# Optimization experiments

Hardware: AMD Instinct MI355X
Metric: run time of the kernel (lower is better)

The kernel has to match this reference:

```python
import jax, jax.numpy as jnp
import numpy as np

B, T, D = 2, 2048, 2048
HK, HV, K, V = 16, 32, 128, 128          # key heads, value heads, head dims
KEY_DIM, VALUE_DIM = HK * K, HV * V      # 2048, 4096
CONV_W = 4                               # causal conv kernel width
EPS = 1e-6


def setup_inputs() -> dict:
    key = jax.random.key(0)
    ks = jax.random.split(key, 8)
    rn = lambda k, shp, sc: jax.random.normal(k, shp, dtype=jnp.float32) * sc
    return {
        "hidden_states": rn(ks[0], (B, T, D), 1.0),
        "W_qkvz": rn(ks[1], (D, 2 * KEY_DIM + 2 * VALUE_DIM), D ** -0.5),
        "W_ba": rn(ks[2], (D, 2 * HV), D ** -0.5),
        "conv_weight": rn(ks[3], (2 * KEY_DIM + VALUE_DIM, CONV_W), CONV_W ** -0.5),
        "A_log": jnp.log(jax.random.uniform(ks[4], (HV,), minval=1.0, maxval=16.0)),
        "dt_bias": rn(ks[5], (HV,), 0.5),
        "norm_weight": jnp.zeros((V,), jnp.float32),  # zero-centered RMSNorm weight
        "W_out": rn(ks[6], (VALUE_DIM, D), VALUE_DIM ** -0.5),
    }


def _l2norm(x):
    return x * jax.lax.rsqrt(jnp.sum(x * x, axis=-1, keepdims=True) + 1e-6)


def _causal_conv_silu(x, w):
    # x: [B,T,C]; depthwise causal conv, kernel width CONV_W, then SiLU
    xp = jnp.pad(x, ((0, 0), (CONV_W - 1, 0), (0, 0)))
    out = sum(xp[:, j:j + x.shape[1], :] * w[None, None, :, j] for j in range(CONV_W))
    return jax.nn.silu(out)


def _gated_delta_rule(q, k, v, g, beta):
    # q,k: [B,T,HV,K] (l2-normed, q pre-scaled); v: [B,T,HV,V]; g,beta: [B,T,HV]
    def step(S, xs):                      # S: [B,HV,K,V]
        q_t, k_t, v_t, g_t, beta_t = xs
        S = S * jnp.exp(g_t)[..., None, None]
        pred = jnp.einsum('bhk,bhkv->bhv', k_t, S)
        delta = (v_t - pred) * beta_t[..., None]
        S = S + jnp.einsum('bhk,bhv->bhkv', k_t, delta)
        o_t = jnp.einsum('bhk,bhkv->bhv', q_t, S)
        return S, o_t

    mv = lambda x: jnp.moveaxis(x, 1, 0)  # time-major for scan
    S0 = jnp.zeros((q.shape[0], HV, K, V), q.dtype)
    _, o = jax.lax.scan(step, S0, (mv(q), mv(k), mv(v), mv(g), mv(beta)))
    return jnp.moveaxis(o, 0, 1)          # [B,T,HV,V]


def reference(hidden_states, W_qkvz, W_ba, conv_weight, A_log, dt_bias,
              norm_weight, W_out):
    b_, t_ = hidden_states.shape[:2]
    qkvz = hidden_states @ W_qkvz
    q, k, v, z = jnp.split(qkvz, [KEY_DIM, 2 * KEY_DIM, 2 * KEY_DIM + VALUE_DIM], axis=-1)
    ba = hidden_states @ W_ba
    b_gate, a = jnp.split(ba, 2, axis=-1)  # each [B,T,HV]

    # fused causal conv1d + SiLU over concat(q,k,v)
    mixed = _causal_conv_silu(jnp.concatenate([q, k, v], axis=-1), conv_weight)
    q, k, v = jnp.split(mixed, [KEY_DIM, 2 * KEY_DIM], axis=-1)

    # gating: beta = sigmoid(b), g = -exp(A_log) * softplus(a + dt_bias)
    beta = jax.nn.sigmoid(b_gate)
    g = -jnp.exp(A_log) * jax.nn.softplus(a + dt_bias)

    # GQA expand (v_per_k_group = HV // HK), l2norm, scale
    rep = HV // HK
    q = jnp.repeat(q.reshape(b_, t_, HK, K), rep, axis=2)
    k = jnp.repeat(k.reshape(b_, t_, HK, K), rep, axis=2)
    v = v.reshape(b_, t_, HV, V)
    q = _l2norm(q) * (K ** -0.5)
    k = _l2norm(k)

    o = _gated_delta_rule(q, k, v, g, beta)  # [B,T,HV,V]

    # gated RMSNorm (per value head, zero-centered weight) then out projection
    zg = z.reshape(b_, t_, HV, V)
    x = o * jax.nn.silu(zg)
    var = jnp.mean(x * x, axis=-1, keepdims=True)
    x = x * jax.lax.rsqrt(var + EPS) * (1.0 + norm_weight)
    return x.reshape(b_, t_, VALUE_DIM) @ W_out
```

## Files before the change

### kernel.cpp

```cpp
#include <hip/hip_runtime.h>

typedef unsigned short u16;
typedef unsigned int u32;

typedef short bf16x8 __attribute__((ext_vector_type(8)));
typedef float f32x4 __attribute__((ext_vector_type(4)));

#define T_SEQ 2048
#define MFMA16(a, b, c) __builtin_amdgcn_mfma_f32_16x16x32_bf16(a, b, c, 0, 0, 0)

__device__ __forceinline__ u16 f2bf(float f) {
    u32 u = __float_as_uint(f);
    u += 0x7fffu + ((u >> 16) & 1u);
    return (u16)(u >> 16);
}
__device__ __forceinline__ float bf2f(u16 s) {
    return __uint_as_float(((u32)s) << 16);
}
__device__ __forceinline__ void g2lds16(const u16* gp, u16* lp) {
    __builtin_amdgcn_global_load_lds((const __attribute__((address_space(1))) void*)gp,
                                     (__attribute__((address_space(3))) void*)lp, 16, 0, 0);
}

__global__ __launch_bounds__(256) void cast_f32_bf16(const float* __restrict__ in,
                                                     u16* __restrict__ out, long n) {
    long i = ((long)blockIdx.x * 256 + threadIdx.x) * 4;
    if (i + 3 < n) {
        float4 v = *(const float4*)&in[i];
        out[i + 0] = f2bf(v.x);
        out[i + 1] = f2bf(v.y);
        out[i + 2] = f2bf(v.z);
        out[i + 3] = f2bf(v.w);
    }
}

__global__ __launch_bounds__(256) void transpose_cast(const float* __restrict__ in,
                                                      u16* __restrict__ out, int R, int C) {
    __shared__ float tile[32][33];
    int c0 = blockIdx.x * 32, r0 = blockIdx.y * 32;
    int tx = threadIdx.x & 31, ty = threadIdx.x >> 5;
#pragma unroll
    for (int rr = 0; rr < 32; rr += 8)
        tile[ty + rr][tx] = in[(long)(r0 + ty + rr) * C + c0 + tx];
    __syncthreads();
#pragma unroll
    for (int rr = 0; rr < 32; rr += 8)
        out[(long)(c0 + ty + rr) * R + r0 + tx] = f2bf(tile[tx][ty + rr]);
}

template <int MODE>
__global__ __launch_bounds__(256) void gemm_bt(const u16* __restrict__ A,
                                               const u16* __restrict__ B, void* __restrict__ C,
                                               void* __restrict__ C2, int M, int N, int K, int lda,
                                               int ldb, int ldc) {
    __shared__ __align__(16) u16 As[128 * 32];
    __shared__ __align__(16) u16 Bs[128 * 32];
    int m0 = blockIdx.x * 128, n0 = blockIdx.y * 128;
    int tid = threadIdx.x;
    int lane = tid & 63, w = tid >> 6;
    int wr = w >> 1, wc = w & 1;
    int quad = lane >> 4, l15 = lane & 15;

    f32x4 acc[4][4];
#pragma unroll
    for (int i = 0; i < 4; i++)
#pragma unroll
        for (int j = 0; j < 4; j++) acc[i][j] = (f32x4){0.f, 0.f, 0.f, 0.f};

    int srow = tid >> 2, sc8 = (tid & 3) * 8;
    const u16* Ag = &A[(long)(m0 + srow) * lda + sc8];
    const u16* Bg = &B[(long)(n0 + srow) * ldb + sc8];

    for (int k0 = 0; k0 < K; k0 += 32) {
        g2lds16(Ag + k0, &As[tid * 8]);
        g2lds16(Ag + (long)64 * lda + k0, &As[(256 + tid) * 8]);
        g2lds16(Bg + k0, &Bs[tid * 8]);
        g2lds16(Bg + (long)64 * ldb + k0, &Bs[(256 + tid) * 8]);
        __syncthreads();
        bf16x8 af[4], bfr[4];
#pragma unroll
        for (int i = 0; i < 4; i++) {
            af[i] = *(const bf16x8*)&As[(wr * 64 + i * 16 + l15) * 32 + quad * 8];
            bfr[i] = *(const bf16x8*)&Bs[(wc * 64 + i * 16 + l15) * 32 + quad * 8];
        }
#pragma unroll
        for (int i = 0; i < 4; i++)
#pragma unroll
            for (int j = 0; j < 4; j++) acc[i][j] = MFMA16(af[i], bfr[j], acc[i][j]);
        __syncthreads();
    }

    if (MODE == 0) {
#pragma unroll
        for (int i = 0; i < 4; i++)
#pragma unroll
            for (int j = 0; j < 4; j++)
#pragma unroll
                for (int r = 0; r < 4; r++) {
                    int row = m0 + wr * 64 + i * 16 + quad * 4 + r;
                    int col = n0 + wc * 64 + j * 16 + l15;
                    ((float*)C)[(long)row * ldc + col] = acc[i][j][r];
                }
    } else {
        u16* Cst = As;
        u16* dst;
        long dldc;
        int ncol0;
        if (MODE == 2 && n0 >= 8192) {
            dst = (u16*)C2;
            dldc = 4096;
            ncol0 = n0 - 8192;
        } else {
            dst = (u16*)C;
            dldc = (MODE == 2) ? 8192 : ldc;
            ncol0 = n0;
        }
#pragma unroll 1
        for (int half = 0; half < 2; half++) {
            __syncthreads();
            if (wc == half) {
#pragma unroll
                for (int i = 0; i < 4; i++)
#pragma unroll
                    for (int j = 0; j < 4; j++)
#pragma unroll
                        for (int r = 0; r < 4; r++) {
                            int row = wr * 64 + i * 16 + quad * 4 + r;
                            int col = j * 16 + l15;
                            u16* base = (row < 64) ? As : Bs;
                            base[(row & 63) * 64 + col] = f2bf(acc[i][j][r]);
                        }
            }
            __syncthreads();
#pragma unroll
            for (int rr = 0; rr < 4; rr++) {
                int row = rr * 32 + (tid >> 3), seg = tid & 7;
                u16* base = (row < 64) ? As : Bs;
                *(uint4*)&dst[(long)(m0 + row) * dldc + ncol0 + half * 64 + seg * 8] =
                    *(uint4*)&base[(row & 63) * 64 + seg * 8];
            }
        }
    }
}

__global__ __launch_bounds__(256) void ba_gemm(const u16* __restrict__ hid,
                                               const u16* __restrict__ WbaT,
                                               const float* __restrict__ A_log,
                                               const float* __restrict__ dt_bias,
                                               float* __restrict__ g, float* __restrict__ beta) {
    __shared__ __align__(16) u16 As2[32 * 32];
    int m0 = blockIdx.x * 32;
    int tid = threadIdx.x, lane = tid & 63, w = tid >> 6;
    int quad = lane >> 4, l15 = lane & 15;
    int trow = w & 1;
    int ctile = (w >> 1) * 2;
    f32x4 acc[2];
    acc[0] = (f32x4){0.f, 0.f, 0.f, 0.f};
    acc[1] = (f32x4){0.f, 0.f, 0.f, 0.f};
    for (int k0 = 0; k0 < 2048; k0 += 32) {
        if (tid < 128) {
            int row = tid >> 2, c8 = (tid & 3) * 8;
            *(uint4*)&As2[row * 32 + c8] = *(const uint4*)&hid[(long)(m0 + row) * 2048 + k0 + c8];
        }
        __syncthreads();
        bf16x8 a = *(const bf16x8*)&As2[(trow * 16 + l15) * 32 + quad * 8];
#pragma unroll
        for (int j = 0; j < 2; j++) {
            bf16x8 b = *(const bf16x8*)&WbaT[(long)((ctile + j) * 16 + l15) * 2048 + k0 + quad * 8];
            acc[j] = MFMA16(a, b, acc[j]);
        }
        __syncthreads();
    }
#pragma unroll
    for (int j = 0; j < 2; j++)
#pragma unroll
        for (int r = 0; r < 4; r++) {
            int tok = m0 + trow * 16 + quad * 4 + r;
            int col = (ctile + j) * 16 + l15;
            float tot = acc[j][r];
            if (col < 32) {
                beta[(long)tok * 32 + col] = 1.f / (1.f + expf(-tot));
            } else {
                int h = col - 32;
                float x = tot + dt_bias[h];
                float sp = (x > 20.f) ? x : log1pf(expf(x));
                g[(long)tok * 32 + h] = -expf(A_log[h]) * sp;
            }
        }
}

__global__ __launch_bounds__(256) void conv_gate(const u16* __restrict__ qkv,
                                                 const float* __restrict__ conv_w,
                                                 u16* __restrict__ qn, u16* __restrict__ kn,
                                                 u16* __restrict__ vc) {
    int tok = blockIdx.x, tid = threadIdx.x;
    int tloc = tok & (T_SEQ - 1);
    __shared__ float mixed[8192];
    __shared__ float sh_norm[32];
    uint4 zero4;
    zero4.x = zero4.y = zero4.z = zero4.w = 0u;
#pragma unroll
    for (int i = 0; i < 4; i++) {
        int c = (i * 256 + tid) * 8;
        long base = (long)tok * 8192 + c;
        uint4 x3 = *(const uint4*)&qkv[base];
        uint4 x2 = (tloc >= 1) ? *(const uint4*)&qkv[base - 8192] : zero4;
        uint4 x1 = (tloc >= 2) ? *(const uint4*)&qkv[base - 16384] : zero4;
        uint4 x0 = (tloc >= 3) ? *(const uint4*)&qkv[base - 24576] : zero4;
        const u16* p0 = (const u16*)&x0;
        const u16* p1 = (const u16*)&x1;
        const u16* p2 = (const u16*)&x2;
        const u16* p3 = (const u16*)&x3;
#pragma unroll
        for (int e = 0; e < 8; e++) {
            float4 wv = *(const float4*)&conv_w[(long)(c + e) * 4];
            float a = bf2f(p0[e]) * wv.x + bf2f(p1[e]) * wv.y + bf2f(p2[e]) * wv.z +
                      bf2f(p3[e]) * wv.w;
            mixed[c + e] = a / (1.f + __expf(-a));
        }
    }
    __syncthreads();
    int grp = tid >> 3, sub = tid & 7;
    float ss = 0.f;
#pragma unroll
    for (int e = 0; e < 16; e++) {
        float v = mixed[grp * 128 + sub * 16 + e];
        ss += v * v;
    }
    ss += __shfl_xor(ss, 4, 8);
    ss += __shfl_xor(ss, 2, 8);
    ss += __shfl_xor(ss, 1, 8);
    if (sub == 0) sh_norm[grp] = rsqrtf(ss + 1e-6f);
    __syncthreads();
#pragma unroll
    for (int i = 0; i < 4; i++) {
        int c = (i * 256 + tid) * 8;
        float nf = (c < 2048) ? sh_norm[c >> 7] * 0.08838834764831845f
                              : ((c < 4096) ? sh_norm[c >> 7] : 1.f);
        u16 ob[8];
#pragma unroll
        for (int e = 0; e < 8; e++) ob[e] = f2bf(mixed[c + e] * nf);
        uint4 val = *(uint4*)ob;
        if (c < 2048)
            *(uint4*)&qn[(long)tok * 2048 + c] = val;
        else if (c < 4096)
            *(uint4*)&kn[(long)tok * 2048 + (c - 2048)] = val;
        else
            *(uint4*)&vc[(long)tok * 4096 + (c - 4096)] = val;
    }
}

__global__ __launch_bounds__(256) void phaseA(const u16* __restrict__ qn,
                                              const u16* __restrict__ kn,
                                              const u16* __restrict__ vc,
                                              const float* __restrict__ g,
                                              const float* __restrict__ beta,
                                              u16* __restrict__ Tv_g, u16* __restrict__ Tw_g,
                                              u16* __restrict__ Q2_g, u16* __restrict__ obuf) {
    __shared__ __align__(16) u16 Yrm[64][256];
    __shared__ __align__(16) float BMt[64][64];
    __shared__ __align__(16) u16 kbuf[64][128];
    u16* Lbf = &kbuf[0][0];

    int bid = blockIdx.x;
    int c = bid & 31, h = (bid >> 5) & 31, b = bid >> 10;
    int hk = h >> 1;
    long tokbase = (long)b * T_SEQ + c * 64;
    long cb = (long)bid * 8192;
    int tid = threadIdx.x, lane = tid & 63, w = tid >> 6;
    int quad = lane >> 4, l15 = lane & 15;

    float gl = g[(tokbase + lane) * 32 + h];
    float bl = beta[(tokbase + lane) * 32 + h];
    float cgl = gl;
#pragma unroll
    for (int d = 1; d < 64; d <<= 1) {
        float y = __shfl_up(cgl, d);
        if (lane >= d) cgl += y;
    }
    float wscl = bl * __expf(cgl);
    float eCgl = __expf(cgl);

#pragma unroll
    for (int p = 0; p < 4; p++) {
        int u = p * 256 + tid;
        int row = u >> 4, col8 = (u & 15) * 8;
        *(uint4*)&kbuf[row][col8] = *(const uint4*)&kn[(tokbase + row) * 2048 + hk * 128 + col8];
    }
    __syncthreads();

    {
        f32x4 gk[4];
#pragma unroll
        for (int nj = 0; nj < 4; nj++) gk[nj] = (f32x4){0.f, 0.f, 0.f, 0.f};
#pragma unroll
        for (int kk = 0; kk < 4; kk++) {
            bf16x8 a = *(const bf16x8*)&kbuf[w * 16 + l15][kk * 32 + quad * 8];
#pragma unroll
            for (int nj = 0; nj < 4; nj++) {
                bf16x8 bb = *(const bf16x8*)&kbuf[nj * 16 + l15][kk * 32 + quad * 8];
                gk[nj] = MFMA16(a, bb, gk[nj]);
            }
        }
#pragma unroll
        for (int nj = 0; nj < 4; nj++)
#pragma unroll
            for (int r = 0; r < 4; r++) {
                int i = w * 16 + quad * 4 + r;
                int j = nj * 16 + l15;
                float cgi = __shfl(cgl, i), cgj = __shfl(cgl, j);
                float bi = __shfl(bl, i);
                BMt[j][i] = (j < i) ? bi * gk[nj][r] * __expf(cgi - cgj) : 0.f;
            }
    }
    __syncthreads();

    {
        int col = tid;
        bool isV = col < 128;
        int kcol = col & 127;
        long vbase = tokbase * 4096 + h * 128 + kcol;
        float Yreg[8], acc8[8];
#pragma unroll 1
        for (int bi = 0; bi < 8; ++bi) {
            float vr[8];
            if (isV) {
#pragma unroll
                for (int ii = 0; ii < 8; ii++)
                    vr[ii] = bf2f(vc[vbase + (long)(bi * 8 + ii) * 4096]);
            }
#pragma unroll
            for (int ii = 0; ii < 8; ii++) acc8[ii] = 0.f;
            for (int j = 0; j < bi * 8; ++j) {
                float yv = bf2f(Yrm[j][col]);
                float4 m0 = *(const float4*)&BMt[j][bi * 8];
                float4 m1 = *(const float4*)&BMt[j][bi * 8 + 4];
                acc8[0] += m0.x * yv;
                acc8[1] += m0.y * yv;
                acc8[2] += m0.z * yv;
                acc8[3] += m0.w * yv;
                acc8[4] += m1.x * yv;
                acc8[5] += m1.y * yv;
                acc8[6] += m1.z * yv;
                acc8[7] += m1.w * yv;
            }
#pragma unroll
            for (int ii = 0; ii < 8; ii++) {
                int i = bi * 8 + ii;
                float rhs = isV ? __shfl(bl, i) * vr[ii] : __shfl(wscl, i) * bf2f(kbuf[i][kcol]);
                float s = rhs - acc8[ii];
#pragma unroll
                for (int jj = 0; jj < 8; jj++)
                    if (jj < ii) s -= BMt[bi * 8 + jj][i] * Yreg[jj];
                Yreg[ii] = s;
                u16 sb = f2bf(s);
                Yrm[i][col] = sb;
                if (isV)
                    Tv_g[cb + i * 128 + kcol] = sb;
                else
                    Tw_g[cb + i * 128 + kcol] = sb;
            }
        }
    }
    __syncthreads();

    {
        f32x4 qk_[4];
#pragma unroll
        for (int nj = 0; nj < 4; nj++) qk_[nj] = (f32x4){0.f, 0.f, 0.f, 0.f};
#pragma unroll
        for (int kk = 0; kk < 4; kk++) {
            bf16x8 a = *(const bf16x8*)&qn[(tokbase + w * 16 + l15) * 2048 + hk * 128 + kk * 32 +
                                           quad * 8];
#pragma unroll
            for (int nj = 0; nj < 4; nj++) {
                bf16x8 bb = *(const bf16x8*)&kbuf[nj * 16 + l15][kk * 32 + quad * 8];
                qk_[nj] = MFMA16(a, bb, qk_[nj]);
            }
        }
        __syncthreads();
#pragma unroll
        for (int nj = 0; nj < 4; nj++)
#pragma unroll
            for (int r = 0; r < 4; r++) {
                int t = w * 16 + quad * 4 + r;
                int rr = nj * 16 + l15;
                float cgt = __shfl(cgl, t), cgr = __shfl(cgl, rr);
                float val = (rr <= t) ? qk_[nj][r] * __expf(cgt - cgr) : 0.f;
                Lbf[t * 64 + rr] = f2bf(val);
            }
    }
    __syncthreads();

#pragma unroll 1
    for (int half = 0; half < 2; half++) {
        f32x4 oa[8];
#pragma unroll
        for (int nj = 0; nj < 8; nj++) oa[nj] = (f32x4){0.f, 0.f, 0.f, 0.f};
#pragma unroll
        for (int kk = 0; kk < 2; kk++) {
            bf16x8 a = *(const bf16x8*)&Lbf[(w * 16 + l15) * 64 + kk * 32 + quad * 8];
#pragma unroll
            for (int nj = 0; nj < 8; nj++) {
                bf16x8 bb;
#pragma unroll
                for (int jj = 0; jj < 8; jj++)
                    bb[jj] = (short)Yrm[kk * 32 + quad * 8 + jj][half * 128 + nj * 16 + l15];
                oa[nj] = MFMA16(a, bb, oa[nj]);
            }
        }
        if (half == 0) {
#pragma unroll
            for (int nj = 0; nj < 8; nj++)
#pragma unroll
                for (int r = 0; r < 4; r++) {
                    int t = w * 16 + quad * 4 + r;
                    int vcol = nj * 16 + l15;
                    obuf[(tokbase + t) * 4096 + h * 128 + vcol] = f2bf(oa[nj][r]);
                }
        } else {
#pragma unroll
            for (int nj = 0; nj < 8; nj++)
#pragma unroll
                for (int r = 0; r < 4; r++) {
                    int t = w * 16 + quad * 4 + r;
                    int kcol = nj * 16 + l15;
                    float qsc = __shfl(eCgl, t);
                    float qv = bf2f(qn[(tokbase + t) * 2048 + hk * 128 + kcol]);
                    Q2_g[cb + t * 128 + kcol] = f2bf(qsc * qv - oa[nj][r]);
                }
        }
    }
}

__global__ __launch_bounds__(256) void phaseB(const u16* __restrict__ kn,
                                              const float* __restrict__ g,
                                              const u16* __restrict__ Tv_g,
                                              const u16* __restrict__ Tw_g,
                                              const u16* __restrict__ Q2_g,
                                              u16* __restrict__ obuf) {
    __shared__ __align__(16) float Sf[128][32];
    __shared__ __align__(16) u16 SbfT[32][128];
    __shared__ __align__(16) u16 KhT[128][64];
    __shared__ __align__(16) u16 Ut[32][64];

    int bid = blockIdx.x;
    int vq = bid & 3, h = (bid >> 2) & 31, b = bid >> 7;
    int hk = h >> 1;
    int tid = threadIdx.x, lane = tid & 63, w = tid >> 6;
    int quad = lane >> 4, l15 = lane & 15;

    for (int p = tid; p < 128 * 32; p += 256) {
        ((float*)Sf)[p] = 0.f;
        ((u16*)SbfT)[p] = 0;
    }
    __syncthreads();

    for (int c = 0; c < 32; ++c) {
        long tokbase = (long)b * T_SEQ + c * 64;
        long cb = (long)(((b * 32 + h) * 32) + c) * 8192;
        float gl = g[(tokbase + lane) * 32 + h];
        float cgl = gl;
#pragma unroll
        for (int d = 1; d < 64; d <<= 1) {
            float y = __shfl_up(cgl, d);
            if (lane >= d) cgl += y;
        }
        float cgC = __shfl(cgl, 63);
        float A_C = __expf(cgC);
        float kscl = __expf(cgC - cgl);

        {
            int s = tid >> 2, qq = tid & 3;
            float ksc = __shfl(kscl, s);
            const u16* kp = &kn[(tokbase + s) * 2048 + hk * 128 + qq * 32];
            u16 tmp[32];
            *(uint4*)&tmp[0] = *(const uint4*)&kp[0];
            *(uint4*)&tmp[8] = *(const uint4*)&kp[8];
            *(uint4*)&tmp[16] = *(const uint4*)&kp[16];
            *(uint4*)&tmp[24] = *(const uint4*)&kp[24];
#pragma unroll
            for (int j = 0; j < 32; j++) KhT[qq * 32 + j][s] = f2bf(bf2f(tmp[j]) * ksc);
        }

        f32x4 y1[2], oo[2];
#pragma unroll
        for (int nj = 0; nj < 2; nj++) {
            y1[nj] = (f32x4){0.f, 0.f, 0.f, 0.f};
            oo[nj] = (f32x4){0.f, 0.f, 0.f, 0.f};
        }
#pragma unroll
        for (int kk = 0; kk < 4; kk++) {
            bf16x8 aTw = *(const bf16x8*)&Tw_g[cb + (w * 16 + l15) * 128 + kk * 32 + quad * 8];
            bf16x8 aQ2 = *(const bf16x8*)&Q2_g[cb + (w * 16 + l15) * 128 + kk * 32 + quad * 8];
#pragma unroll
            for (int nj = 0; nj < 2; nj++) {
                bf16x8 bb = *(const bf16x8*)&SbfT[nj * 16 + l15][kk * 32 + quad * 8];
                y1[nj] = MFMA16(aTw, bb, y1[nj]);
                oo[nj] = MFMA16(aQ2, bb, oo[nj]);
            }
        }
#pragma unroll
        for (int nj = 0; nj < 2; nj++)
#pragma unroll
            for (int r = 0; r < 4; r++) {
                int i = w * 16 + quad * 4 + r;
                int vl = nj * 16 + l15;
                int vg = vq * 32 + vl;
                float tvv = bf2f(Tv_g[cb + (long)i * 128 + vg]);
                Ut[vl][i] = f2bf(tvv - y1[nj][r]);
                long op = (tokbase + i) * 4096 + h * 128 + vg;
                obuf[op] = f2bf(bf2f(obuf[op]) + oo[nj][r]);
            }
        __syncthreads();

#pragma unroll
        for (int mm = 0; mm < 2; mm++) {
            int mi = 2 * w + mm;
#pragma unroll
            for (int nj = 0; nj < 2; nj++) {
                f32x4 sacc;
#pragma unroll
                for (int r = 0; r < 4; r++)
                    sacc[r] = A_C * Sf[mi * 16 + quad * 4 + r][nj * 16 + l15];
#pragma unroll
                for (int kk = 0; kk < 2; kk++) {
                    bf16x8 a = *(const bf16x8*)&KhT[mi * 16 + l15][kk * 32 + quad * 8];
                    bf16x8 bb = *(const bf16x8*)&Ut[nj * 16 + l15][kk * 32 + quad * 8];
                    sacc = MFMA16(a, bb, sacc);
                }
#pragma unroll
                for (int r = 0; r < 4; r++) {
                    int kd = mi * 16 + quad * 4 + r, vl = nj * 16 + l15;
                    Sf[kd][vl] = sacc[r];
                    SbfT[vl][kd] = f2bf(sacc[r]);
                }
            }
        }
        __syncthreads();
    }
}

__global__ __launch_bounds__(256) void gated_norm(const u16* __restrict__ obuf,
                                                  const u16* __restrict__ zbuf,
                                                  const float* __restrict__ norm_w,
                                                  u16* __restrict__ xn) {
    int tok = blockIdx.x, tid = threadIdx.x;
    long obase = (long)tok * 4096 + tid * 16;
    u16 ob[16], zb[16];
    *(uint4*)(ob + 0) = *(const uint4*)&obuf[obase];
    *(uint4*)(ob + 8) = *(const uint4*)&obuf[obase + 8];
    *(uint4*)(zb + 0) = *(const uint4*)&zbuf[obase];
    *(uint4*)(zb + 8) = *(const uint4*)&zbuf[obase + 8];
    float x[16];
    float ss = 0.f;
#pragma unroll
    for (int i = 0; i < 16; i++) {
        float ov = bf2f(ob[i]);
        float zv = bf2f(zb[i]);
        float xv = ov * (zv / (1.f + expf(-zv)));
        x[i] = xv;
        ss += xv * xv;
    }
    ss += __shfl_xor(ss, 4, 8);
    ss += __shfl_xor(ss, 2, 8);
    ss += __shfl_xor(ss, 1, 8);
    float scale = rsqrtf(ss * (1.f / 128.f) + 1e-6f);
    int cbase = (tid * 16) & 127;
#pragma unroll
    for (int i = 0; i < 16; i++)
        xn[(long)tok * 4096 + tid * 16 + i] = f2bf(x[i] * scale * (1.f + norm_w[cbase + i]));
}

extern "C" void kernel_launch(void* const* d_in, const int* in_sizes, int n_in, void* d_out,
                              int out_size, void* d_ws, size_t ws_size, hipStream_t stream) {
    const float* hidden = (const float*)d_in[0];
    const float* W_qkvz = (const float*)d_in[1];
    const float* W_ba = (const float*)d_in[2];
    const float* conv_w = (const float*)d_in[3];
    const float* A_log = (const float*)d_in[4];
    const float* dt_bias = (const float*)d_in[5];
    const float* norm_w = (const float*)d_in[6];
    const float* W_out = (const float*)d_in[7];
    float* out = (float*)d_out;

    char* ws = (char*)d_ws;
    u16* wqT = (u16*)(ws + 0);
    u16* qn = (u16*)(ws + 0);
    u16* vc = (u16*)(ws + 16777216L);
    u16* hidbf = (u16*)(ws + 50331648L);
    u16* kn = (u16*)(ws + 50331648L);
    u16* woT = (u16*)(ws + 67108864L);
    u16* qkv_raw = (u16*)(ws + 83886080L);
    u16* Tv = (u16*)(ws + 83886080L);
    u16* Tw = (u16*)(ws + 117440512L);
    u16* xn = (u16*)(ws + 83886080L);
    u16* WbaT = (u16*)(ws + 150994944L);
    u16* zbuf = (u16*)(ws + 150994944L);
    u16* Q2 = (u16*)(ws + 184549376L);
    float* g = (float*)(ws + 218103808L);
    float* beta = (float*)(ws + 218628096L);
    u16* obuf = vc;

    cast_f32_bf16<<<8192, 256, 0, stream>>>(hidden, hidbf, 8388608L);
    transpose_cast<<<dim3(384, 64), 256, 0, stream>>>(W_qkvz, wqT, 2048, 12288);
    transpose_cast<<<dim3(64, 128), 256, 0, stream>>>(W_out, woT, 4096, 2048);
    transpose_cast<<<dim3(2, 64), 256, 0, stream>>>(W_ba, WbaT, 2048, 64);
    ba_gemm<<<128, 256, 0, stream>>>(hidbf, WbaT, A_log, dt_bias, g, beta);
    gemm_bt<2><<<dim3(32, 96), 256, 0, stream>>>(hidbf, wqT, qkv_raw, zbuf, 4096, 12288, 2048,
                                                 2048, 2048, 0);
    conv_gate<<<4096, 256, 0, stream>>>(qkv_raw, conv_w, qn, kn, vc);
    phaseA<<<2048, 256, 0, stream>>>(qn, kn, vc, g, beta, Tv, Tw, Q2, obuf);
    phaseB<<<256, 256, 0, stream>>>(kn, g, Tv, Tw, Q2, obuf);
    gated_norm<<<4096, 256, 0, stream>>>(obuf, zbuf, norm_w, xn);
    gemm_bt<0><<<dim3(32, 16), 256, 0, stream>>>(xn, woT, out, nullptr, 4096, 2048, 4096, 4096,
                                                 4096, 2048);
}
```

Baseline: 1.120 ms.

## Use 32x32 MFMA in GEMM, stage ba weights in LDS, prefetch phaseB chunks

The main GEMM switches from 16x16x32 to 32x32x16 bf16 MFMA tiles, so each wave issues fewer instructions per tile and reuses each fragment load more. The ba projection now stages its weight tile in LDS instead of each wave reading it from global memory. In the recurrent phaseB kernel, the global loads for the next chunk (g, k, Tw, Q2, Tv, the old output) are issued before the state-update MFMAs, hiding memory latency behind the sequential recurrence. phaseB's LDS arrays are padded to reduce bank conflicts. The cost is higher register pressure from the prefetch buffers.

Result: faster. 1.038 ms (-7.3%).

```diff
diff --git a/kernel.cpp b/kernel.cpp
--- a/kernel.cpp
+++ b/kernel.cpp
@@ -5,9 +5,11 @@
 
 typedef short bf16x8 __attribute__((ext_vector_type(8)));
 typedef float f32x4 __attribute__((ext_vector_type(4)));
+typedef float f32x16 __attribute__((ext_vector_type(16)));
 
 #define T_SEQ 2048
 #define MFMA16(a, b, c) __builtin_amdgcn_mfma_f32_16x16x32_bf16(a, b, c, 0, 0, 0)
+#define MFMA32(a, b, c) __builtin_amdgcn_mfma_f32_32x32x16_bf16(a, b, c, 0, 0, 0)
 
 __device__ __forceinline__ u16 f2bf(float f) {
     u32 u = __float_as_uint(f);
@@ -59,13 +61,15 @@
     int tid = threadIdx.x;
     int lane = tid & 63, w = tid >> 6;
     int wr = w >> 1, wc = w & 1;
-    int quad = lane >> 4, l15 = lane & 15;
-
-    f32x4 acc[4][4];
-#pragma unroll
-    for (int i = 0; i < 4; i++)
-#pragma unroll
-        for (int j = 0; j < 4; j++) acc[i][j] = (f32x4){0.f, 0.f, 0.f, 0.f};
+    int l31 = lane & 31, hf = lane >> 5;
+
+    f32x16 acc[2][2];
+#pragma unroll
+    for (int mi = 0; mi < 2; mi++)
+#pragma unroll
+        for (int nj = 0; nj < 2; nj++)
+#pragma unroll
+            for (int r = 0; r < 16; r++) acc[mi][nj][r] = 0.f;
 
     int srow = tid >> 2, sc8 = (tid & 3) * 8;
     const u16* Ag = &A[(long)(m0 + srow) * lda + sc8];
@@ -77,32 +81,37 @@
         g2lds16(Bg + k0, &Bs[tid * 8]);
         g2lds16(Bg + (long)64 * ldb + k0, &Bs[(256 + tid) * 8]);
         __syncthreads();
-        bf16x8 af[4], bfr[4];
-#pragma unroll
-        for (int i = 0; i < 4; i++) {
-            af[i] = *(const bf16x8*)&As[(wr * 64 + i * 16 + l15) * 32 + quad * 8];
-            bfr[i] = *(const bf16x8*)&Bs[(wc * 64 + i * 16 + l15) * 32 + quad * 8];
-        }
-#pragma unroll
-        for (int i = 0; i < 4; i++)
-#pragma unroll
-            for (int j = 0; j < 4; j++) acc[i][j] = MFMA16(af[i], bfr[j], acc[i][j]);
+        bf16x8 af[2][2], bfr[2][2];
+#pragma unroll
+        for (int mi = 0; mi < 2; mi++)
+#pragma unroll
+            for (int ks = 0; ks < 2; ks++) {
+                af[mi][ks] = *(const bf16x8*)&As[(wr * 64 + mi * 32 + l31) * 32 + ks * 16 + hf * 8];
+                bfr[mi][ks] =
+                    *(const bf16x8*)&Bs[(wc * 64 + mi * 32 + l31) * 32 + ks * 16 + hf * 8];
+            }
+#pragma unroll
+        for (int ks = 0; ks < 2; ks++)
+#pragma unroll
+            for (int mi = 0; mi < 2; mi++)
+#pragma unroll
+                for (int nj = 0; nj < 2; nj++)
+                    acc[mi][nj] = MFMA32(af[mi][ks], bfr[nj][ks], acc[mi][nj]);
         __syncthreads();
     }
 
     if (MODE == 0) {
 #pragma unroll
-        for (int i = 0; i < 4; i++)
-#pragma unroll
-            for (int j = 0; j < 4; j++)
-#pragma unroll
-                for (int r = 0; r < 4; r++) {
-                    int row = m0 + wr * 64 + i * 16 + quad * 4 + r;
-                    int col = n0 + wc * 64 + j * 16 + l15;
-                    ((float*)C)[(long)row * ldc + col] = acc[i][j][r];
+        for (int mi = 0; mi < 2; mi++)
+#pragma unroll
+            for (int nj = 0; nj < 2; nj++)
+#pragma unroll
+                for (int r = 0; r < 16; r++) {
+                    int row = m0 + wr * 64 + mi * 32 + (r >> 2) * 8 + hf * 4 + (r & 3);
+                    int col = n0 + wc * 64 + nj * 32 + l31;
+                    ((float*)C)[(long)row * ldc + col] = acc[mi][nj][r];
                 }
     } else {
-        u16* Cst = As;
         u16* dst;
         long dldc;
         int ncol0;
@@ -116,19 +125,19 @@
             ncol0 = n0;
         }
 #pragma unroll 1
-        for (int half = 0; half < 2; half++) {
+        for (int half_e = 0; half_e < 2; half_e++) {
             __syncthreads();
-            if (wc == half) {
-#pragma unroll
-                for (int i = 0; i < 4; i++)
-#pragma unroll
-                    for (int j = 0; j < 4; j++)
-#pragma unroll
-                        for (int r = 0; r < 4; r++) {
-                            int row = wr * 64 + i * 16 + quad * 4 + r;
-                            int col = j * 16 + l15;
+            if (wc == half_e) {
+#pragma unroll
+                for (int mi = 0; mi < 2; mi++)
+#pragma unroll
+                    for (int nj = 0; nj < 2; nj++)
+#pragma unroll
+                        for (int r = 0; r < 16; r++) {
+                            int row = wr * 64 + mi * 32 + (r >> 2) * 8 + hf * 4 + (r & 3);
+                            int col = nj * 32 + l31;
                             u16* base = (row < 64) ? As : Bs;
-                            base[(row & 63) * 64 + col] = f2bf(acc[i][j][r]);
+                            base[(row & 63) * 64 + col] = f2bf(acc[mi][nj][r]);
                         }
             }
             __syncthreads();
@@ -136,7 +145,7 @@
             for (int rr = 0; rr < 4; rr++) {
                 int row = rr * 32 + (tid >> 3), seg = tid & 7;
                 u16* base = (row < 64) ? As : Bs;
-                *(uint4*)&dst[(long)(m0 + row) * dldc + ncol0 + half * 64 + seg * 8] =
+                *(uint4*)&dst[(long)(m0 + row) * dldc + ncol0 + half_e * 64 + seg * 8] =
                     *(uint4*)&base[(row & 63) * 64 + seg * 8];
             }
         }
@@ -149,6 +158,7 @@
                                                const float* __restrict__ dt_bias,
                                                float* __restrict__ g, float* __restrict__ beta) {
     __shared__ __align__(16) u16 As2[32 * 32];
+    __shared__ __align__(16) u16 Bs2[64 * 32];
     int m0 = blockIdx.x * 32;
     int tid = threadIdx.x, lane = tid & 63, w = tid >> 6;
     int quad = lane >> 4, l15 = lane & 15;
@@ -157,16 +167,16 @@
     f32x4 acc[2];
     acc[0] = (f32x4){0.f, 0.f, 0.f, 0.f};
     acc[1] = (f32x4){0.f, 0.f, 0.f, 0.f};
+    int srow = tid >> 2, sc8 = (tid & 3) * 8;
     for (int k0 = 0; k0 < 2048; k0 += 32) {
-        if (tid < 128) {
-            int row = tid >> 2, c8 = (tid & 3) * 8;
-            *(uint4*)&As2[row * 32 + c8] = *(const uint4*)&hid[(long)(m0 + row) * 2048 + k0 + c8];
-        }
+        if (tid < 128)
+            *(uint4*)&As2[srow * 32 + sc8] = *(const uint4*)&hid[(long)(m0 + srow) * 2048 + k0 + sc8];
+        *(uint4*)&Bs2[srow * 32 + sc8] = *(const uint4*)&WbaT[(long)srow * 2048 + k0 + sc8];
         __syncthreads();
         bf16x8 a = *(const bf16x8*)&As2[(trow * 16 + l15) * 32 + quad * 8];
 #pragma unroll
         for (int j = 0; j < 2; j++) {
-            bf16x8 b = *(const bf16x8*)&WbaT[(long)((ctile + j) * 16 + l15) * 2048 + k0 + quad * 8];
+            bf16x8 b = *(const bf16x8*)&Bs2[((ctile + j) * 16 + l15) * 32 + quad * 8];
             acc[j] = MFMA16(a, b, acc[j]);
         }
         __syncthreads();
@@ -440,9 +450,9 @@
                                               const u16* __restrict__ Q2_g,
                                               u16* __restrict__ obuf) {
     __shared__ __align__(16) float Sf[128][32];
-    __shared__ __align__(16) u16 SbfT[32][128];
-    __shared__ __align__(16) u16 KhT[128][64];
-    __shared__ __align__(16) u16 Ut[32][64];
+    __shared__ __align__(16) u16 SbfT[32][136];
+    __shared__ __align__(16) u16 KhT[128][72];
+    __shared__ __align__(16) u16 Ut[32][72];
 
     int bid = blockIdx.x;
     int vq = bid & 3, h = (bid >> 2) & 31, b = bid >> 7;
@@ -450,17 +460,43 @@
     int tid = threadIdx.x, lane = tid & 63, w = tid >> 6;
     int quad = lane >> 4, l15 = lane & 15;
 
-    for (int p = tid; p < 128 * 32; p += 256) {
-        ((float*)Sf)[p] = 0.f;
-        ((u16*)SbfT)[p] = 0;
-    }
-    __syncthreads();
+    for (int p = tid; p < 128 * 32; p += 256) ((float*)Sf)[p] = 0.f;
+    for (int p = tid; p < 32 * 136; p += 256) ((u16*)SbfT)[p] = 0;
+    __syncthreads();
+
+    float gl_pf;
+    uint4 kreg[4];
+    bf16x8 aTw[4], aQ2[4];
+    u16 tvv_pf[2][4], oold[2][4];
+
+#define PB_PREFETCH(cc)                                                                      \
+    {                                                                                        \
+        long tb_ = (long)b * T_SEQ + (cc) * 64;                                              \
+        long cb_ = ((long)((b * 32 + h) * 32) + (cc)) * 8192;                                \
+        gl_pf = g[(tb_ + lane) * 32 + h];                                                    \
+        const u16* kp_ = &kn[(tb_ + lane) * 2048 + hk * 128 + w * 32];                       \
+        kreg[0] = *(const uint4*)&kp_[0];                                                    \
+        kreg[1] = *(const uint4*)&kp_[8];                                                    \
+        kreg[2] = *(const uint4*)&kp_[16];                                                   \
+        kreg[3] = *(const uint4*)&kp_[24];                                                   \
+        _Pragma("unroll") for (int kk = 0; kk < 4; kk++) {                                   \
+            aTw[kk] = *(const bf16x8*)&Tw_g[cb_ + (w * 16 + l15) * 128 + kk * 32 + quad * 8]; \
+            aQ2[kk] = *(const bf16x8*)&Q2_g[cb_ + (w * 16 + l15) * 128 + kk * 32 + quad * 8]; \
+        }                                                                                    \
+        _Pragma("unroll") for (int nj = 0; nj < 2; nj++) _Pragma("unroll")                   \
+            for (int r = 0; r < 4; r++) {                                                    \
+            int i_ = w * 16 + quad * 4 + r;                                                  \
+            int vg_ = vq * 32 + nj * 16 + l15;                                               \
+            tvv_pf[nj][r] = Tv_g[cb_ + (long)i_ * 128 + vg_];                                \
+            oold[nj][r] = obuf[(tb_ + i_) * 4096 + h * 128 + vg_];                           \
+        }                                                                                    \
+    }
+
+    PB_PREFETCH(0);
 
     for (int c = 0; c < 32; ++c) {
         long tokbase = (long)b * T_SEQ + c * 64;
-        long cb = (long)(((b * 32 + h) * 32) + c) * 8192;
-        float gl = g[(tokbase + lane) * 32 + h];
-        float cgl = gl;
+        float cgl = gl_pf;
 #pragma unroll
         for (int d = 1; d < 64; d <<= 1) {
             float y = __shfl_up(cgl, d);
@@ -471,16 +507,9 @@
         float kscl = __expf(cgC - cgl);
 
         {
-            int s = tid >> 2, qq = tid & 3;
-            float ksc = __shfl(kscl, s);
-            const u16* kp = &kn[(tokbase + s) * 2048 + hk * 128 + qq * 32];
-            u16 tmp[32];
-            *(uint4*)&tmp[0] = *(const uint4*)&kp[0];
-            *(uint4*)&tmp[8] = *(const uint4*)&kp[8];
-            *(uint4*)&tmp[16] = *(const uint4*)&kp[16];
-            *(uint4*)&tmp[24] = *(const uint4*)&kp[24];
-#pragma unroll
-            for (int j = 0; j < 32; j++) KhT[qq * 32 + j][s] = f2bf(bf2f(tmp[j]) * ksc);
+            const u16* kk16 = (const u16*)kreg;
+#pragma unroll
+            for (int j = 0; j < 32; j++) KhT[w * 32 + j][lane] = f2bf(bf2f(kk16[j]) * kscl);
         }
 
         f32x4 y1[2], oo[2];
@@ -491,13 +520,11 @@
         }
 #pragma unroll
         for (int kk = 0; kk < 4; kk++) {
-            bf16x8 aTw = *(const bf16x8*)&Tw_g[cb + (w * 16 + l15) * 128 + kk * 32 + quad * 8];
-            bf16x8 aQ2 = *(const bf16x8*)&Q2_g[cb + (w * 16 + l15) * 128 + kk * 32 + quad * 8];
 #pragma unroll
             for (int nj = 0; nj < 2; nj++) {
                 bf16x8 bb = *(const bf16x8*)&SbfT[nj * 16 + l15][kk * 32 + quad * 8];
-                y1[nj] = MFMA16(aTw, bb, y1[nj]);
-                oo[nj] = MFMA16(aQ2, bb, oo[nj]);
+                y1[nj] = MFMA16(aTw[kk], bb, y1[nj]);
+                oo[nj] = MFMA16(aQ2[kk], bb, oo[nj]);
             }
         }
 #pragma unroll
@@ -507,12 +534,13 @@
                 int i = w * 16 + quad * 4 + r;
                 int vl = nj * 16 + l15;
                 int vg = vq * 32 + vl;
-                float tvv = bf2f(Tv_g[cb + (long)i * 128 + vg]);
-                Ut[vl][i] = f2bf(tvv - y1[nj][r]);
-                long op = (tokbase + i) * 4096 + h * 128 + vg;
-                obuf[op] = f2bf(bf2f(obuf[op]) + oo[nj][r]);
+                Ut[vl][i] = f2bf(bf2f(tvv_pf[nj][r]) - y1[nj][r]);
+                obuf[(tokbase + i) * 4096 + h * 128 + vg] =
+                    f2bf(bf2f(oold[nj][r]) + oo[nj][r]);
             }
         __syncthreads();
+
+        if (c + 1 < 32) PB_PREFETCH(c + 1);
 
 #pragma unroll
         for (int mm = 0; mm < 2; mm++) {
@@ -539,6 +567,7 @@
         }
         __syncthreads();
     }
+#undef PB_PREFETCH
 }
 
 __global__ __launch_bounds__(256) void gated_norm(const u16* __restrict__ obuf,
```
